# Kernel optimization log

Measured on AMD Instinct MI355X. Metric: run time of the kernel, lower is better.

The kernel has to match this reference:

```python
import jax, jax.numpy as jnp
import numpy as np

N = 50000      # num nodes
E = 600000     # num edges
D = 128        # num_node_features (in == out)
R = 8          # num_relations


def setup_inputs() -> dict:
    key = jax.random.key(0)
    k = jax.random.split(key, 6)
    x = jax.random.normal(k[0], (N, D), dtype=jnp.float32)
    edge_index = jax.random.randint(k[1], (2, E), 0, N, dtype=jnp.int32)
    edge_type = jax.random.randint(k[2], (E,), 0, R, dtype=jnp.int32)
    scale = 1.0 / np.sqrt(D).astype(np.float32)
    weight = jax.random.normal(k[3], (R, D, D), dtype=jnp.float32) * scale  # per-relation W_r
    root = jax.random.normal(k[4], (D, D), dtype=jnp.float32) * scale       # self-loop weight
    bias = jnp.zeros((D,), dtype=jnp.float32)
    return {"x": x, "edge_index": edge_index, "edge_type": edge_type,
            "weight": weight, "root": root, "bias": bias}


def _rgcn(x, weight, root, bias, edge_index, edge_type):
    # RGCNConv (PyG defaults: aggr='mean' per relation, root weight + bias)
    src, dst = edge_index[0], edge_index[1]
    # combined segment id over (relation, dst) so one segment_sum covers all relations
    seg = edge_type * N + dst                              # [E]
    msgs = x[src]                                          # [E, D] gather
    sums = jax.ops.segment_sum(msgs, seg, num_segments=R * N)                 # [R*N, D]
    cnts = jax.ops.segment_sum(jnp.ones((E, 1), x.dtype), seg, num_segments=R * N)
    mean = sums / jnp.maximum(cnts, 1.0)                   # mean over neighbors, 0 if none
    agg = mean.reshape(R, N, D)
    out = jnp.einsum('rnd,rde->ne', agg, weight) + x @ root + bias
    return out


def reference(x, edge_index, edge_type, weight, root, bias):
    return jax.nn.relu(_rgcn(x, weight, root, bias, edge_index, edge_type))
```

## Files before the change

kernel.cpp:

```cpp
#include <hip/hip_runtime.h>

constexpr int NN = 50000;
constexpr int NE = 600000;
constexpr int D  = 128;
constexpr int NR = 8;
constexpr int KT = (NR + 1) * D;

constexpr int SCAN_ELEMS = 1024;
constexpr int NBLK_SCAN  = (NN + SCAN_ELEMS - 1) / SCAN_ELEMS;

typedef unsigned int   u32;
typedef unsigned short u16;
typedef float  f32x4 __attribute__((ext_vector_type(4)));
typedef short  s16x8 __attribute__((ext_vector_type(8)));

__device__ __forceinline__ u16 f2bf(float f) {
    u32 u = __float_as_uint(f);
    u32 r = (u + 0x7fffu + ((u >> 16) & 1u)) >> 16;
    return (u16)r;
}

__device__ __forceinline__ void async_cp16(const void* g, void* l) {
    __builtin_amdgcn_global_load_lds(
        (const __attribute__((address_space(1))) u32*)g,
        (__attribute__((address_space(3))) u32*)l, 16, 0, 0);
}

__global__ __launch_bounds__(256) void count_dst(const int* __restrict__ dst,
                                                 int* __restrict__ cnt_d) {
    int e = blockIdx.x * 256 + threadIdx.x;
    if (e < NE) atomicAdd(&cnt_d[dst[e]], 1);
}

__global__ __launch_bounds__(256) void scan1(const int* __restrict__ cnt,
                                             int* __restrict__ offs,
                                             int* __restrict__ bsums) {
    __shared__ int lds[256];
    int t = threadIdx.x;
    int base = blockIdx.x * SCAN_ELEMS + t * 4;
    int v0 = (base + 0 < NN) ? cnt[base + 0] : 0;
    int v1 = (base + 1 < NN) ? cnt[base + 1] : 0;
    int v2 = (base + 2 < NN) ? cnt[base + 2] : 0;
    int v3 = (base + 3 < NN) ? cnt[base + 3] : 0;
    int s = v0 + v1 + v2 + v3;
    lds[t] = s;
    __syncthreads();
    int val = s;
    for (int off = 1; off < 256; off <<= 1) {
        int tmp = (t >= off) ? lds[t - off] : 0;
        __syncthreads();
        val += tmp;
        lds[t] = val;
        __syncthreads();
    }
    int ex = val - s;
    if (base + 0 < NN) offs[base + 0] = ex;
    if (base + 1 < NN) offs[base + 1] = ex + v0;
    if (base + 2 < NN) offs[base + 2] = ex + v0 + v1;
    if (base + 3 < NN) offs[base + 3] = ex + v0 + v1 + v2;
    if (t == 255) bsums[blockIdx.x] = val;
}

__global__ __launch_bounds__(64) void scan2(int* __restrict__ bsums) {
    __shared__ int lds[64];
    int t = threadIdx.x;
    int v = (t < NBLK_SCAN) ? bsums[t] : 0;
    lds[t] = v;
    __syncthreads();
    int val = v;
    for (int off = 1; off < 64; off <<= 1) {
        int tmp = (t >= off) ? lds[t - off] : 0;
        __syncthreads();
        val += tmp;
        lds[t] = val;
        __syncthreads();
    }
    if (t < NBLK_SCAN) bsums[t] = val - v;
}

__global__ __launch_bounds__(256) void scan3(int* __restrict__ offs,
                                             const int* __restrict__ bsums) {
    int i = blockIdx.x * 256 + threadIdx.x;
    if (i < NN) offs[i] += bsums[i >> 10];
    if (i == 0) offs[NN] = NE;
}

__global__ __launch_bounds__(256) void fill_bins(const int* __restrict__ src,
                                                 const int* __restrict__ dst,
                                                 const int* __restrict__ et,
                                                 int* __restrict__ cur,
                                                 int* __restrict__ ebin) {
    int e = blockIdx.x * 256 + threadIdx.x;
    if (e >= NE) return;
    int idx = atomicAdd(&cur[dst[e]], 1);
    ebin[idx] = (et[e] << 16) | src[e];
}

__global__ __launch_bounds__(256) void convert_x(const float* __restrict__ x,
                                                 u16* __restrict__ xb) {
    int i = (blockIdx.x * 256 + threadIdx.x) * 4;
    if (i >= NN * D) return;
    float4 v = *(const float4*)(x + i);
    ushort4 o;
    o.x = f2bf(v.x); o.y = f2bf(v.y); o.z = f2bf(v.z); o.w = f2bf(v.w);
    *(ushort4*)(xb + i) = o;
}

__global__ __launch_bounds__(256) void transpose_w(const float* __restrict__ weight,
                                                   const float* __restrict__ root,
                                                   u16* __restrict__ wt,
                                                   u16* __restrict__ rt) {
    int gid = blockIdx.x * 256 + threadIdx.x;
    if (gid >= (NR + 1) * D * D) return;
    int p = gid >> 14;
    int idx = gid & 16383;
    int n = idx >> 7, k = idx & 127;
    float v = (p < NR) ? weight[(size_t)p * D * D + k * D + n] : root[k * D + n];
    u16* dst = (p < NR) ? (wt + (size_t)p * D * D) : rt;
    dst[idx] = f2bf(v);
}

__global__ __launch_bounds__(128) void aggregate_kernel(const u32* __restrict__ xw,
                                                        const int* __restrict__ offs,
                                                        const int* __restrict__ ebin,
                                                        u32* __restrict__ sw) {
    const int lane = threadIdx.x & 63;
    const int n = blockIdx.x * 2 + (threadIdx.x >> 6);
    if (n >= NN) return;
    const int beg = __builtin_amdgcn_readfirstlane(offs[n]);
    const int c   = __builtin_amdgcn_readfirstlane(offs[n + 1]) - beg;

    float acc[NR][2];
    int cnt[NR];
#pragma unroll
    for (int r = 0; r < NR; ++r) { acc[r][0] = 0.f; acc[r][1] = 0.f; cnt[r] = 0; }

    int q0 = 0, q1 = 0, q2 = 0, q3 = 0, q4 = 0, q5 = 0, q6 = 0, q7 = 0;
    u32 v0 = 0, v1 = 0, v2 = 0, v3 = 0, v4 = 0, v5 = 0, v6 = 0, v7 = 0;

#define REFILL(Q, V, IDX)                                                   \
    if ((IDX) < c) {                                                        \
        Q = __builtin_amdgcn_readfirstlane(ebin[beg + (IDX)]);              \
        V = xw[(size_t)((u32)Q & 0xffffu) * 64 + lane];                     \
    }
#define CONSUME(Q, V)                                                       \
    {                                                                       \
        float lo_ = __uint_as_float((V) << 16);                             \
        float hi_ = __uint_as_float((V) & 0xffff0000u);                     \
        switch ((u32)(Q) >> 16) {                                           \
        case 0: acc[0][0] += lo_; acc[0][1] += hi_; ++cnt[0]; break;        \
        case 1: acc[1][0] += lo_; acc[1][1] += hi_; ++cnt[1]; break;        \
        case 2: acc[2][0] += lo_; acc[2][1] += hi_; ++cnt[2]; break;        \
        case 3: acc[3][0] += lo_; acc[3][1] += hi_; ++cnt[3]; break;        \
        case 4: acc[4][0] += lo_; acc[4][1] += hi_; ++cnt[4]; break;        \
        case 5: acc[5][0] += lo_; acc[5][1] += hi_; ++cnt[5]; break;        \
        case 6: acc[6][0] += lo_; acc[6][1] += hi_; ++cnt[6]; break;        \
        default: acc[7][0] += lo_; acc[7][1] += hi_; ++cnt[7]; break;       \
        }                                                                   \
    }

    REFILL(q0, v0, 0) REFILL(q1, v1, 1) REFILL(q2, v2, 2) REFILL(q3, v3, 3)
    REFILL(q4, v4, 4) REFILL(q5, v5, 5) REFILL(q6, v6, 6) REFILL(q7, v7, 7)

    int e = 0;
    for (; e + 8 <= c; e += 8) {
        CONSUME(q0, v0) REFILL(q0, v0, e + 8)
        CONSUME(q1, v1) REFILL(q1, v1, e + 9)
        CONSUME(q2, v2) REFILL(q2, v2, e + 10)
        CONSUME(q3, v3) REFILL(q3, v3, e + 11)
        CONSUME(q4, v4) REFILL(q4, v4, e + 12)
        CONSUME(q5, v5) REFILL(q5, v5, e + 13)
        CONSUME(q6, v6) REFILL(q6, v6, e + 14)
        CONSUME(q7, v7) REFILL(q7, v7, e + 15)
    }
    if (e + 0 < c) CONSUME(q0, v0)
    if (e + 1 < c) CONSUME(q1, v1)
    if (e + 2 < c) CONSUME(q2, v2)
    if (e + 3 < c) CONSUME(q3, v3)
    if (e + 4 < c) CONSUME(q4, v4)
    if (e + 5 < c) CONSUME(q5, v5)
    if (e + 6 < c) CONSUME(q6, v6)
    if (e + 7 < c) CONSUME(q7, v7)
#undef REFILL
#undef CONSUME

#pragma unroll
    for (int r = 0; r < NR; ++r) {
        float inv = 1.0f / (float)(cnt[r] > 0 ? cnt[r] : 1);
        u32 lo16 = f2bf(acc[r][0] * inv);
        u32 hi16 = f2bf(acc[r][1] * inv);
        sw[((size_t)r * NN + n) * 64 + lane] = lo16 | (hi16 << 16);
    }
}

__global__ __launch_bounds__(256) void mfma_gemm(const u16* __restrict__ xb,
                                                 const u16* __restrict__ sums,
                                                 const u16* __restrict__ rt,
                                                 const u16* __restrict__ wt,
                                                 const float* __restrict__ bias,
                                                 float* __restrict__ out) {
    __shared__ u16 As[128 * 32];
    __shared__ u16 Bs[128 * 32];

    const int tid  = threadIdx.x;
    const int wave = tid >> 6;
    const int lane = tid & 63;
    const int wm   = (wave & 1) * 64;
    const int wn   = (wave >> 1) * 64;
    const int m0   = blockIdx.x * 128;

    f32x4 acc[4][4];
#pragma unroll
    for (int i = 0; i < 4; ++i)
#pragma unroll
        for (int j = 0; j < 4; ++j) acc[i][j] = (f32x4){0.f, 0.f, 0.f, 0.f};

    for (int k0 = 0; k0 < KT; k0 += 32) {
        const int rpl = k0 >> 7;
        const int kof = k0 & 127;
        const u16* Ap = (rpl == 0) ? xb : sums + (size_t)(rpl - 1) * NN * D;
        const u16* Bp = (rpl == 0) ? rt : wt + (size_t)(rpl - 1) * D * D;

        __syncthreads();
#pragma unroll
        for (int j = 0; j < 2; ++j) {
            int row = wave * 32 + j * 16 + (lane >> 2);
            int ga  = m0 + row; if (ga > NN - 1) ga = NN - 1;
            async_cp16(Ap + (size_t)ga * D + kof + (lane & 3) * 8,
                       &As[(wave * 32 + j * 16) * 32]);
            async_cp16(Bp + (size_t)row * D + kof + (lane & 3) * 8,
                       &Bs[(wave * 32 + j * 16) * 32]);
        }
        __syncthreads();

        s16x8 af[4], bf[4];
        const int fr = lane & 15;
        const int fk = (lane >> 4) * 8;
#pragma unroll
        for (int mt = 0; mt < 4; ++mt)
            af[mt] = *(const s16x8*)&As[(wm + mt * 16 + fr) * 32 + fk];
#pragma unroll
        for (int nt = 0; nt < 4; ++nt)
            bf[nt] = *(const s16x8*)&Bs[(wn + nt * 16 + fr) * 32 + fk];
#pragma unroll
        for (int mt = 0; mt < 4; ++mt)
#pragma unroll
            for (int nt = 0; nt < 4; ++nt)
                acc[mt][nt] = __builtin_amdgcn_mfma_f32_16x16x32_bf16(
                    af[mt], bf[nt], acc[mt][nt], 0, 0, 0);
    }

    const int cl = lane & 15;
    const int rq = (lane >> 4) * 4;
#pragma unroll
    for (int nt = 0; nt < 4; ++nt) {
        int col = wn + nt * 16 + cl;
        float bv = bias[col];
#pragma unroll
        for (int mt = 0; mt < 4; ++mt) {
#pragma unroll
            for (int reg = 0; reg < 4; ++reg) {
                int n = m0 + wm + mt * 16 + rq + reg;
                if (n < NN) {
                    float v = acc[mt][nt][reg] + bv;
                    out[(size_t)n * D + col] = fmaxf(v, 0.0f);
                }
            }
        }
    }
}

extern "C" void kernel_launch(void* const* d_in, const int* in_sizes, int n_in,
                              void* d_out, int out_size, void* d_ws, size_t ws_size,
                              hipStream_t stream) {
    const float* x      = (const float*)d_in[0];
    const int*   ei     = (const int*)d_in[1];
    const int*   et     = (const int*)d_in[2];
    const float* weight = (const float*)d_in[3];
    const float* root   = (const float*)d_in[4];
    const float* bias   = (const float*)d_in[5];
    float* out = (float*)d_out;
    const int* srcv = ei;
    const int* dstv = ei + NE;

    int* cnt_d = (int*)d_ws;
    int* cur   = cnt_d + NN;
    int* offs  = cur + NN;
    int* bsums = offs + NN + 1;
    int* ebin  = bsums + 64;
    size_t fixed_b  = ((char*)(ebin + NE) - (char*)d_ws);
    size_t fixed_al = (fixed_b + 255) & ~(size_t)255;
    u16* xb   = (u16*)((char*)d_ws + fixed_al);
    u16* sums = xb + (size_t)NN * D;
    u16* wt   = sums + (size_t)NR * NN * D;
    u16* rt   = wt + (size_t)NR * D * D;

    hipMemsetAsync(cnt_d, 0, NN * sizeof(int), stream);
    count_dst<<<(NE + 255) / 256, 256, 0, stream>>>(dstv, cnt_d);
    scan1<<<NBLK_SCAN, 256, 0, stream>>>(cnt_d, offs, bsums);
    scan2<<<1, 64, 0, stream>>>(bsums);
    scan3<<<(NN + 255) / 256, 256, 0, stream>>>(offs, bsums);
    hipMemcpyAsync(cur, offs, NN * sizeof(int), hipMemcpyDeviceToDevice, stream);
    fill_bins<<<(NE + 255) / 256, 256, 0, stream>>>(srcv, dstv, et, cur, ebin);

    convert_x<<<(NN * D / 4 + 255) / 256, 256, 0, stream>>>(x, xb);
    transpose_w<<<((NR + 1) * D * D + 255) / 256, 256, 0, stream>>>(weight, root, wt, rt);

    aggregate_kernel<<<(NN + 1) / 2, 128, 0, stream>>>((const u32*)xb, offs, ebin, (u32*)sums);

    mfma_gemm<<<(NN + 127) / 128, 256, 0, stream>>>(xb, sums, rt, wt, bias, out);
}
```

Measured before the change: 266.9 us.

## Fuse prep kernels, sort edges by (dst,relation), and retile GEMM to 64 rows

The x conversion, weight transpose and edge counting now run in one launch, and the edges are counted and binned per (dst, relation) segment so each node's edges arrive sorted by relation. The aggregate kernel then keeps a single running accumulator and flushes each relation's mean in turn, replacing the eight-way per-edge switch and its register-heavy accumulator array. The memcpy into the cursor array is folded into scan3. The GEMM moves to 64-row tiles where each wave covers all 128 columns, which doubles the block count. The cost is a scan over a segment array eight times larger and a flush loop with data-dependent branching.

```diff
diff --git a/kernel.cpp b/kernel.cpp
--- a/kernel.cpp
+++ b/kernel.cpp
@@ -5,9 +5,10 @@
 constexpr int D  = 128;
 constexpr int NR = 8;
 constexpr int KT = (NR + 1) * D;
+constexpr int NSEG = NN * NR;
 
 constexpr int SCAN_ELEMS = 1024;
-constexpr int NBLK_SCAN  = (NN + SCAN_ELEMS - 1) / SCAN_ELEMS;
+constexpr int NBLK2 = (NSEG + SCAN_ELEMS - 1) / SCAN_ELEMS;
 
 typedef unsigned int   u32;
 typedef unsigned short u16;
@@ -26,10 +27,38 @@
         (__attribute__((address_space(3))) u32*)l, 16, 0, 0);
 }
 
-__global__ __launch_bounds__(256) void count_dst(const int* __restrict__ dst,
-                                                 int* __restrict__ cnt_d) {
-    int e = blockIdx.x * 256 + threadIdx.x;
-    if (e < NE) atomicAdd(&cnt_d[dst[e]], 1);
+__global__ __launch_bounds__(256) void prep_all(const float* __restrict__ x,
+                                                const float* __restrict__ weight,
+                                                const float* __restrict__ root,
+                                                const int* __restrict__ dst,
+                                                const int* __restrict__ et,
+                                                u16* __restrict__ xb,
+                                                u16* __restrict__ wt,
+                                                u16* __restrict__ rt,
+                                                int* __restrict__ cnt2) {
+    const int NX4 = NN * D / 4;
+    const int NW  = (NR + 1) * D * D;
+    int gid = blockIdx.x * 256 + threadIdx.x;
+    if (gid < NX4) {
+        int i = gid * 4;
+        float4 v = *(const float4*)(x + i);
+        ushort4 o;
+        o.x = f2bf(v.x); o.y = f2bf(v.y); o.z = f2bf(v.z); o.w = f2bf(v.w);
+        *(ushort4*)(xb + i) = o;
+        return;
+    }
+    int g = gid - NX4;
+    if (g < NW) {
+        int p = g >> 14;
+        int idx = g & 16383;
+        int n = idx >> 7, k = idx & 127;
+        float v = (p < NR) ? weight[(size_t)p * D * D + k * D + n] : root[k * D + n];
+        u16* dp = (p < NR) ? (wt + (size_t)p * D * D) : rt;
+        dp[idx] = f2bf(v);
+        return;
+    }
+    int e = g - NW;
+    if (e < NE) atomicAdd(&cnt2[dst[e] * NR + et[e]], 1);
 }
 
 __global__ __launch_bounds__(256) void scan1(const int* __restrict__ cnt,
@@ -38,10 +67,10 @@
     __shared__ int lds[256];
     int t = threadIdx.x;
     int base = blockIdx.x * SCAN_ELEMS + t * 4;
-    int v0 = (base + 0 < NN) ? cnt[base + 0] : 0;
-    int v1 = (base + 1 < NN) ? cnt[base + 1] : 0;
-    int v2 = (base + 2 < NN) ? cnt[base + 2] : 0;
-    int v3 = (base + 3 < NN) ? cnt[base + 3] : 0;
+    int v0 = (base + 0 < NSEG) ? cnt[base + 0] : 0;
+    int v1 = (base + 1 < NSEG) ? cnt[base + 1] : 0;
+    int v2 = (base + 2 < NSEG) ? cnt[base + 2] : 0;
+    int v3 = (base + 3 < NSEG) ? cnt[base + 3] : 0;
     int s = v0 + v1 + v2 + v3;
     lds[t] = s;
     __syncthreads();
@@ -54,35 +83,40 @@
         __syncthreads();
     }
     int ex = val - s;
-    if (base + 0 < NN) offs[base + 0] = ex;
-    if (base + 1 < NN) offs[base + 1] = ex + v0;
-    if (base + 2 < NN) offs[base + 2] = ex + v0 + v1;
-    if (base + 3 < NN) offs[base + 3] = ex + v0 + v1 + v2;
+    if (base + 0 < NSEG) offs[base + 0] = ex;
+    if (base + 1 < NSEG) offs[base + 1] = ex + v0;
+    if (base + 2 < NSEG) offs[base + 2] = ex + v0 + v1;
+    if (base + 3 < NSEG) offs[base + 3] = ex + v0 + v1 + v2;
     if (t == 255) bsums[blockIdx.x] = val;
 }
 
-__global__ __launch_bounds__(64) void scan2(int* __restrict__ bsums) {
-    __shared__ int lds[64];
+__global__ __launch_bounds__(512) void scan2(int* __restrict__ bsums) {
+    __shared__ int lds[512];
     int t = threadIdx.x;
-    int v = (t < NBLK_SCAN) ? bsums[t] : 0;
+    int v = (t < NBLK2) ? bsums[t] : 0;
     lds[t] = v;
     __syncthreads();
     int val = v;
-    for (int off = 1; off < 64; off <<= 1) {
+    for (int off = 1; off < 512; off <<= 1) {
         int tmp = (t >= off) ? lds[t - off] : 0;
         __syncthreads();
         val += tmp;
         lds[t] = val;
         __syncthreads();
     }
-    if (t < NBLK_SCAN) bsums[t] = val - v;
+    if (t < NBLK2) bsums[t] = val - v;
 }
 
 __global__ __launch_bounds__(256) void scan3(int* __restrict__ offs,
+                                             int* __restrict__ cur,
                                              const int* __restrict__ bsums) {
     int i = blockIdx.x * 256 + threadIdx.x;
-    if (i < NN) offs[i] += bsums[i >> 10];
-    if (i == 0) offs[NN] = NE;
+    if (i < NSEG) {
+        int v = offs[i] + bsums[i >> 10];
+        offs[i] = v;
+        cur[i]  = v;
+    }
+    if (i == 0) offs[NSEG] = NE;
 }
 
 __global__ __launch_bounds__(256) void fill_bins(const int* __restrict__ src,
@@ -92,48 +126,23 @@
                                                  int* __restrict__ ebin) {
     int e = blockIdx.x * 256 + threadIdx.x;
     if (e >= NE) return;
-    int idx = atomicAdd(&cur[dst[e]], 1);
-    ebin[idx] = (et[e] << 16) | src[e];
-}
-
-__global__ __launch_bounds__(256) void convert_x(const float* __restrict__ x,
-                                                 u16* __restrict__ xb) {
-    int i = (blockIdx.x * 256 + threadIdx.x) * 4;
-    if (i >= NN * D) return;
-    float4 v = *(const float4*)(x + i);
-    ushort4 o;
-    o.x = f2bf(v.x); o.y = f2bf(v.y); o.z = f2bf(v.z); o.w = f2bf(v.w);
-    *(ushort4*)(xb + i) = o;
-}
-
-__global__ __launch_bounds__(256) void transpose_w(const float* __restrict__ weight,
-                                                   const float* __restrict__ root,
-                                                   u16* __restrict__ wt,
-                                                   u16* __restrict__ rt) {
-    int gid = blockIdx.x * 256 + threadIdx.x;
-    if (gid >= (NR + 1) * D * D) return;
-    int p = gid >> 14;
-    int idx = gid & 16383;
-    int n = idx >> 7, k = idx & 127;
-    float v = (p < NR) ? weight[(size_t)p * D * D + k * D + n] : root[k * D + n];
-    u16* dst = (p < NR) ? (wt + (size_t)p * D * D) : rt;
-    dst[idx] = f2bf(v);
+    int r = et[e];
+    int idx = atomicAdd(&cur[dst[e] * NR + r], 1);
+    ebin[idx] = (r << 16) | src[e];
 }
 
 __global__ __launch_bounds__(128) void aggregate_kernel(const u32* __restrict__ xw,
-                                                        const int* __restrict__ offs,
+                                                        const int* __restrict__ offs2,
                                                         const int* __restrict__ ebin,
                                                         u32* __restrict__ sw) {
     const int lane = threadIdx.x & 63;
     const int n = blockIdx.x * 2 + (threadIdx.x >> 6);
     if (n >= NN) return;
-    const int beg = __builtin_amdgcn_readfirstlane(offs[n]);
-    const int c   = __builtin_amdgcn_readfirstlane(offs[n + 1]) - beg;
-
-    float acc[NR][2];
-    int cnt[NR];
-#pragma unroll
-    for (int r = 0; r < NR; ++r) { acc[r][0] = 0.f; acc[r][1] = 0.f; cnt[r] = 0; }
+    const int beg = __builtin_amdgcn_readfirstlane(offs2[n * NR]);
+    const int c   = __builtin_amdgcn_readfirstlane(offs2[n * NR + NR]) - beg;
+
+    float a0 = 0.f, a1 = 0.f;
+    int r_cur = 0, cnt_cur = 0;
 
     int q0 = 0, q1 = 0, q2 = 0, q3 = 0, q4 = 0, q5 = 0, q6 = 0, q7 = 0;
     u32 v0 = 0, v1 = 0, v2 = 0, v3 = 0, v4 = 0, v5 = 0, v6 = 0, v7 = 0;
@@ -143,20 +152,21 @@
         Q = __builtin_amdgcn_readfirstlane(ebin[beg + (IDX)]);              \
         V = xw[(size_t)((u32)Q & 0xffffu) * 64 + lane];                     \
     }
+#define FLUSH()                                                             \
+    {                                                                       \
+        float inv_ = 1.0f / (float)(cnt_cur > 0 ? cnt_cur : 1);             \
+        u32 lo16_ = f2bf(a0 * inv_);                                        \
+        u32 hi16_ = f2bf(a1 * inv_);                                        \
+        sw[((size_t)r_cur * NN + n) * 64 + lane] = lo16_ | (hi16_ << 16);   \
+        a0 = 0.f; a1 = 0.f; cnt_cur = 0; ++r_cur;                           \
+    }
 #define CONSUME(Q, V)                                                       \
     {                                                                       \
-        float lo_ = __uint_as_float((V) << 16);                             \
-        float hi_ = __uint_as_float((V) & 0xffff0000u);                     \
-        switch ((u32)(Q) >> 16) {                                           \
-        case 0: acc[0][0] += lo_; acc[0][1] += hi_; ++cnt[0]; break;        \
-        case 1: acc[1][0] += lo_; acc[1][1] += hi_; ++cnt[1]; break;        \
-        case 2: acc[2][0] += lo_; acc[2][1] += hi_; ++cnt[2]; break;        \
-        case 3: acc[3][0] += lo_; acc[3][1] += hi_; ++cnt[3]; break;        \
-        case 4: acc[4][0] += lo_; acc[4][1] += hi_; ++cnt[4]; break;        \
-        case 5: acc[5][0] += lo_; acc[5][1] += hi_; ++cnt[5]; break;        \
-        case 6: acc[6][0] += lo_; acc[6][1] += hi_; ++cnt[6]; break;        \
-        default: acc[7][0] += lo_; acc[7][1] += hi_; ++cnt[7]; break;       \
-        }                                                                   \
+        int rj_ = (int)((u32)(Q) >> 16);                                    \
+        while (r_cur < rj_) FLUSH()                                         \
+        a0 += __uint_as_float((V) << 16);                                   \
+        a1 += __uint_as_float((V) & 0xffff0000u);                           \
+        ++cnt_cur;                                                          \
     }
 
     REFILL(q0, v0, 0) REFILL(q1, v1, 1) REFILL(q2, v2, 2) REFILL(q3, v3, 3)
@@ -181,16 +191,11 @@
     if (e + 5 < c) CONSUME(q5, v5)
     if (e + 6 < c) CONSUME(q6, v6)
     if (e + 7 < c) CONSUME(q7, v7)
+
+    while (r_cur < NR) FLUSH()
 #undef REFILL
+#undef FLUSH
 #undef CONSUME
-
-#pragma unroll
-    for (int r = 0; r < NR; ++r) {
-        float inv = 1.0f / (float)(cnt[r] > 0 ? cnt[r] : 1);
-        u32 lo16 = f2bf(acc[r][0] * inv);
-        u32 hi16 = f2bf(acc[r][1] * inv);
-        sw[((size_t)r * NN + n) * 64 + lane] = lo16 | (hi16 << 16);
-    }
 }
 
 __global__ __launch_bounds__(256) void mfma_gemm(const u16* __restrict__ xb,
@@ -199,21 +204,20 @@
                                                  const u16* __restrict__ wt,
                                                  const float* __restrict__ bias,
                                                  float* __restrict__ out) {
-    __shared__ u16 As[128 * 32];
+    __shared__ u16 As[64 * 32];
     __shared__ u16 Bs[128 * 32];
 
     const int tid  = threadIdx.x;
     const int wave = tid >> 6;
     const int lane = tid & 63;
-    const int wm   = (wave & 1) * 64;
-    const int wn   = (wave >> 1) * 64;
-    const int m0   = blockIdx.x * 128;
-
-    f32x4 acc[4][4];
+    const int m0   = blockIdx.x * 64;
+
+    f32x4 acc[8];
 #pragma unroll
-    for (int i = 0; i < 4; ++i)
-#pragma unroll
-        for (int j = 0; j < 4; ++j) acc[i][j] = (f32x4){0.f, 0.f, 0.f, 0.f};
+    for (int j = 0; j < 8; ++j) acc[j] = (f32x4){0.f, 0.f, 0.f, 0.f};
+
+    const int srow = 16 * wave + (lane >> 2);
+    const int sch  = (lane & 3) * 8;
 
     for (int k0 = 0; k0 < KT; k0 += 32) {
         const int rpl = k0 >> 7;
@@ -222,49 +226,37 @@
         const u16* Bp = (rpl == 0) ? rt : wt + (size_t)(rpl - 1) * D * D;
 
         __syncthreads();
-#pragma unroll
-        for (int j = 0; j < 2; ++j) {
-            int row = wave * 32 + j * 16 + (lane >> 2);
-            int ga  = m0 + row; if (ga > NN - 1) ga = NN - 1;
-            async_cp16(Ap + (size_t)ga * D + kof + (lane & 3) * 8,
-                       &As[(wave * 32 + j * 16) * 32]);
-            async_cp16(Bp + (size_t)row * D + kof + (lane & 3) * 8,
-                       &Bs[(wave * 32 + j * 16) * 32]);
+        {
+            int ga = m0 + srow; if (ga > NN - 1) ga = NN - 1;
+            async_cp16(Ap + (size_t)ga * D + kof + sch, (char*)As + wave * 1024);
+            async_cp16(Bp + (size_t)srow * D + kof + sch, (char*)Bs + wave * 1024);
+            async_cp16(Bp + (size_t)(64 + srow) * D + kof + sch,
+                       (char*)Bs + 4096 + wave * 1024);
         }
         __syncthreads();
 
-        s16x8 af[4], bf[4];
         const int fr = lane & 15;
         const int fk = (lane >> 4) * 8;
+        s16x8 af = *(const s16x8*)&As[(16 * wave + fr) * 32 + fk];
 #pragma unroll
-        for (int mt = 0; mt < 4; ++mt)
-            af[mt] = *(const s16x8*)&As[(wm + mt * 16 + fr) * 32 + fk];
-#pragma unroll
-        for (int nt = 0; nt < 4; ++nt)
-            bf[nt] = *(const s16x8*)&Bs[(wn + nt * 16 + fr) * 32 + fk];
-#pragma unroll
-        for (int mt = 0; mt < 4; ++mt)
-#pragma unroll
-            for (int nt = 0; nt < 4; ++nt)
-                acc[mt][nt] = __builtin_amdgcn_mfma_f32_16x16x32_bf16(
-                    af[mt], bf[nt], acc[mt][nt], 0, 0, 0);
+        for (int nt = 0; nt < 8; ++nt) {
+            s16x8 bf = *(const s16x8*)&Bs[(nt * 16 + fr) * 32 + fk];
+            acc[nt] = __builtin_amdgcn_mfma_f32_16x16x32_bf16(af, bf, acc[nt], 0, 0, 0);
+        }
     }
 
     const int cl = lane & 15;
     const int rq = (lane >> 4) * 4;
 #pragma unroll
-    for (int nt = 0; nt < 4; ++nt) {
-        int col = wn + nt * 16 + cl;
+    for (int nt = 0; nt < 8; ++nt) {
+        int col = nt * 16 + cl;
         float bv = bias[col];
 #pragma unroll
-        for (int mt = 0; mt < 4; ++mt) {
-#pragma unroll
-            for (int reg = 0; reg < 4; ++reg) {
-                int n = m0 + wm + mt * 16 + rq + reg;
-                if (n < NN) {
-                    float v = acc[mt][nt][reg] + bv;
-                    out[(size_t)n * D + col] = fmaxf(v, 0.0f);
-                }
+        for (int reg = 0; reg < 4; ++reg) {
+            int n = m0 + 16 * wave + rq + reg;
+            if (n < NN) {
+                float v = acc[nt][reg] + bv;
+                out[(size_t)n * D + col] = fmaxf(v, 0.0f);
             }
         }
     }
@@ -283,11 +275,11 @@
     const int* srcv = ei;
     const int* dstv = ei + NE;
 
-    int* cnt_d = (int*)d_ws;
-    int* cur   = cnt_d + NN;
-    int* offs  = cur + NN;
-    int* bsums = offs + NN + 1;
-    int* ebin  = bsums + 64;
+    int* cnt2  = (int*)d_ws;
+    int* cur2  = cnt2 + NSEG;
+    int* offs2 = cur2 + NSEG;
+    int* bsums = offs2 + NSEG + 1;
+    int* ebin  = bsums + 512;
     size_t fixed_b  = ((char*)(ebin + NE) - (char*)d_ws);
     size_t fixed_al = (fixed_b + 255) & ~(size_t)255;
     u16* xb   = (u16*)((char*)d_ws + fixed_al);
@@ -295,18 +287,19 @@
     u16* wt   = sums + (size_t)NR * NN * D;
     u16* rt   = wt + (size_t)NR * D * D;
 
-    hipMemsetAsync(cnt_d, 0, NN * sizeof(int), stream);
-    count_dst<<<(NE + 255) / 256, 256, 0, stream>>>(dstv, cnt_d);
-    scan1<<<NBLK_SCAN, 256, 0, stream>>>(cnt_d, offs, bsums);
-    scan2<<<1, 64, 0, stream>>>(bsums);
-    scan3<<<(NN + 255) / 256, 256, 0, stream>>>(offs, bsums);
-    hipMemcpyAsync(cur, offs, NN * sizeof(int), hipMemcpyDeviceToDevice, stream);
-    fill_bins<<<(NE + 255) / 256, 256, 0, stream>>>(srcv, dstv, et, cur, ebin);
-
-    convert_x<<<(NN * D / 4 + 255) / 256, 256, 0, stream>>>(x, xb);
-    transpose_w<<<((NR + 1) * D * D + 255) / 256, 256, 0, stream>>>(weight, root, wt, rt);
-
-    aggregate_kernel<<<(NN + 1) / 2, 128, 0, stream>>>((const u32*)xb, offs, ebin, (u32*)sums);
-
-    mfma_gemm<<<(NN + 127) / 128, 256, 0, stream>>>(xb, sums, rt, wt, bias, out);
-}
+    hipMemsetAsync(cnt2, 0, NSEG * sizeof(int), stream);
+
+    const int PREP = NN * D / 4 + (NR + 1) * D * D + NE;
+    prep_all<<<(PREP + 255) / 256, 256, 0, stream>>>(x, weight, root, dstv, et,
+                                                     xb, wt, rt, cnt2);
+
+    scan1<<<NBLK2, 256, 0, stream>>>(cnt2, offs2, bsums);
+    scan2<<<1, 512, 0, stream>>>(bsums);
+    scan3<<<(NSEG + 256) / 256, 256, 0, stream>>>(offs2, cur2, bsums);
+    fill_bins<<<(NE + 255) / 256, 256, 0, stream>>>(srcv, dstv, et, cur2, ebin);
+
+    aggregate_kernel<<<(NN + 1) / 2, 128, 0, stream>>>((const u32*)xb, offs2, ebin,
+                                                       (u32*)sums);
+
+    mfma_gemm<<<(NN + 63) / 64, 256, 0, stream>>>(xb, sums, rt, wt, bias, out);
+}
```

Result: faster. 220.0 us (-17.6%).
